# Optimization experiments

Measured on AMD Instinct MI355X. Metric: run time of the kernel, lower is better.

The kernel has to match this reference:

```python
import jax, jax.numpy as jnp
import numpy as np

N_NODES = 100000


def _gcn_layer(h, W, b, src, dst, norm, n):
    # h: [N, Fin] -> transform then normalized scatter-add aggregation
    h = h @ W                                   # [N, Fout]
    msg = h[src] * norm[:, None]                # [E', Fout] gather + scale
    out = jax.ops.segment_sum(msg, dst, num_segments=n)  # scatter-add
    return out + b


def setup_inputs() -> dict:
    key = jax.random.key(0)
    k1, k2, k3, k4 = jax.random.split(key, 4)
    N, F_IN, HID, C, E = N_NODES, 512, 128, 40, 1600000
    x = jax.random.normal(k1, (N, F_IN), dtype=jnp.float32)
    edge_index = jax.random.randint(k2, (2, E), 0, N, dtype=jnp.int64)
    W1 = jax.random.normal(k3, (F_IN, HID), dtype=jnp.float32) * (1.0 / np.sqrt(F_IN))
    b1 = jnp.zeros((HID,), dtype=jnp.float32)
    W2 = jax.random.normal(k4, (HID, C), dtype=jnp.float32) * (1.0 / np.sqrt(HID))
    b2 = jnp.zeros((C,), dtype=jnp.float32)
    return {"x": x, "edge_index": edge_index, "W1": W1, "b1": b1, "W2": W2, "b2": b2}


def reference(x, edge_index, W1, b1, W2, b2):
    n = x.shape[0]
    # add self-loops (GCNConv default)
    loop = jnp.arange(n, dtype=edge_index.dtype)
    src = jnp.concatenate([edge_index[0], loop])
    dst = jnp.concatenate([edge_index[1], loop])
    # symmetric normalization: deg counted on destination (in-degree, incl. self-loop)
    deg = jax.ops.segment_sum(jnp.ones_like(dst, dtype=x.dtype), dst, num_segments=n)
    dis = jnp.where(deg > 0, jax.lax.rsqrt(deg), 0.0)  # deg^{-1/2}
    norm = dis[src] * dis[dst]                          # per-edge weight

    h = jax.nn.relu(_gcn_layer(x, W1, b1, src, dst, norm, n))
    # dropout: identity in eval mode (training=False)
    h = _gcn_layer(h, W2, b2, src, dst, norm, n)
    return jax.nn.log_softmax(h, axis=1)
```

## Files before the change

### kernel.cpp

```cpp
#include <hip/hip_runtime.h>
#include <hip/hip_bf16.h>


#define F_IN 512
#define HID  128
#define NC   40

typedef __attribute__((ext_vector_type(8))) short bf16x8;
typedef __attribute__((ext_vector_type(4))) float f32x4v;

__device__ __forceinline__ ushort f2bf(float f) {
    union { float f; unsigned u; } x; x.f = f;
    unsigned r = x.u + 0x7FFFu + ((x.u >> 16) & 1u);
    return (ushort)(r >> 16);
}
__device__ __forceinline__ float bf2f(ushort u) {
    return __uint_as_float((unsigned)u << 16);
}

__global__ void count_deg(const int* __restrict__ dst, int E, unsigned* __restrict__ cnt) {
    int t = blockIdx.x * blockDim.x + threadIdx.x;
    if (t < E) atomicAdd(&cnt[dst[t]], 1u);
}

__global__ __launch_bounds__(1024) void scan_block(const unsigned* __restrict__ cnt,
                                                   unsigned* __restrict__ offs,
                                                   unsigned* __restrict__ bsums,
                                                   float* __restrict__ dis, int N) {
    __shared__ unsigned s[1024];
    int tid = threadIdx.x;
    int i = blockIdx.x * 1024 + tid;
    unsigned v = (i < N) ? cnt[i] : 0u;
    if (i < N) dis[i] = rsqrtf((float)v + 1.0f);
    s[tid] = v;
    __syncthreads();
    #pragma unroll
    for (int d = 1; d < 1024; d <<= 1) {
        unsigned t = (tid >= d) ? s[tid - d] : 0u;
        __syncthreads();
        s[tid] += t;
        __syncthreads();
    }
    if (i < N) offs[i] = s[tid] - v;
    if (tid == 1023) bsums[blockIdx.x] = s[1023];
}

__global__ __launch_bounds__(1024) void scan_bsums(unsigned* __restrict__ bsums, int nb) {
    __shared__ unsigned s[1024];
    int tid = threadIdx.x;
    unsigned v = (tid < nb) ? bsums[tid] : 0u;
    s[tid] = v;
    __syncthreads();
    #pragma unroll
    for (int d = 1; d < 1024; d <<= 1) {
        unsigned t = (tid >= d) ? s[tid - d] : 0u;
        __syncthreads();
        s[tid] += t;
        __syncthreads();
    }
    if (tid < nb) bsums[tid] = s[tid] - v;
}

__global__ __launch_bounds__(1024) void scan_add(unsigned* __restrict__ offs,
                                                 const unsigned* __restrict__ bsums,
                                                 int N, unsigned total) {
    int i = blockIdx.x * 1024 + threadIdx.x;
    if (i < N) offs[i] += bsums[blockIdx.x];
    if (i == 0) offs[N] = total;
}

__global__ void fill_csr(const int* __restrict__ src, const int* __restrict__ dst,
                         const unsigned* __restrict__ offs, unsigned* __restrict__ cursor,
                         int* __restrict__ col, int E) {
    int t = blockIdx.x * blockDim.x + threadIdx.x;
    if (t >= E) return;
    int s = src[t], d = dst[t];
    unsigned pos = offs[d] + atomicAdd(&cursor[d], 1u);
    col[pos] = s;
}

__global__ void packW(const float* __restrict__ W1, const float* __restrict__ W2,
                      ushort* __restrict__ W1p, ushort* __restrict__ W2p) {
    int t = blockIdx.x * 256 + threadIdx.x;
    if (t < 65536) {
        int j = t & 7, n = (t >> 3) & 127, kb = (t >> 10) & 3, s = t >> 12;
        int k = s * 32 + kb * 8 + j;
        W1p[t] = f2bf(W1[(size_t)k * HID + n]);
    } else {
        int q = t - 65536;
        if (q < 6144) {
            int j = q & 7;
            int i2 = q >> 3;
            int n = i2 % 48;
            int i3 = i2 / 48;
            int kb = i3 & 3, ks = i3 >> 2;
            int k = ks * 32 + kb * 8 + j;
            float v = (n < NC) ? W2[(size_t)k * NC + n] : 0.f;
            W2p[q] = f2bf(v);
        }
    }
}

__global__ __launch_bounds__(256) void gemm1_mfma(const float* __restrict__ A,
                                                  const ushort* __restrict__ Bp,
                                                  const float* __restrict__ dis,
                                                  ushort* __restrict__ C, int N) {
    __shared__ __align__(16) ushort As[2][64 * 40];
    __shared__ __align__(16) ushort Bs[2][4096];
    const int tid  = threadIdx.x;
    const int wave = tid >> 6;
    const int lane = tid & 63;
    const int quad = lane >> 4;
    const int mr   = lane & 15;
    const int bm   = blockIdx.x * 64;

    const int sr = tid >> 2;
    const int sq = tid & 3;
    const bool srow_ok = (bm + sr) < N;
    const float* aptr = A + (size_t)(bm + sr) * F_IN + sq * 8;

    f32x4v acc[8];
    #pragma unroll
    for (int t = 0; t < 8; t++) acc[t] = (f32x4v){0.f, 0.f, 0.f, 0.f};

    float4 av0, av1;
    uint4  bv0, bv1;
    const float4 z4 = make_float4(0.f, 0.f, 0.f, 0.f);

    av0 = srow_ok ? *(const float4*)(aptr)     : z4;
    av1 = srow_ok ? *(const float4*)(aptr + 4) : z4;
    bv0 = ((const uint4*)Bp)[tid];
    bv1 = ((const uint4*)Bp)[tid + 256];
    {
        __align__(16) ushort ta[8];
        ta[0]=f2bf(av0.x); ta[1]=f2bf(av0.y); ta[2]=f2bf(av0.z); ta[3]=f2bf(av0.w);
        ta[4]=f2bf(av1.x); ta[5]=f2bf(av1.y); ta[6]=f2bf(av1.z); ta[7]=f2bf(av1.w);
        *(uint4*)&As[0][sr * 40 + sq * 8] = *(const uint4*)ta;
        ((uint4*)Bs[0])[tid] = bv0;
        ((uint4*)Bs[0])[tid + 256] = bv1;
    }
    __syncthreads();

    for (int s = 0; s < 16; s++) {
        if (s < 15) {
            av0 = srow_ok ? *(const float4*)(aptr + (s + 1) * 32)     : z4;
            av1 = srow_ok ? *(const float4*)(aptr + (s + 1) * 32 + 4) : z4;
            const uint4* bp = (const uint4*)(Bp + (size_t)(s + 1) * 4096);
            bv0 = bp[tid];
            bv1 = bp[tid + 256];
        }
        {
            const ushort* ab = As[s & 1];
            const ushort* bb = Bs[s & 1] + quad * 1024;
            bf16x8 a = *(const bf16x8*)&ab[(wave * 16 + mr) * 40 + quad * 8];
            #pragma unroll
            for (int t = 0; t < 8; t++) {
                bf16x8 b = *(const bf16x8*)&bb[(t * 16 + mr) * 8];
                acc[t] = __builtin_amdgcn_mfma_f32_16x16x32_bf16(a, b, acc[t], 0, 0, 0);
            }
        }
        if (s < 15) {
            __align__(16) ushort ta[8];
            ta[0]=f2bf(av0.x); ta[1]=f2bf(av0.y); ta[2]=f2bf(av0.z); ta[3]=f2bf(av0.w);
            ta[4]=f2bf(av1.x); ta[5]=f2bf(av1.y); ta[6]=f2bf(av1.z); ta[7]=f2bf(av1.w);
            int nb = (s + 1) & 1;
            *(uint4*)&As[nb][sr * 40 + sq * 8] = *(const uint4*)ta;
            ((uint4*)Bs[nb])[tid] = bv0;
            ((uint4*)Bs[nb])[tid + 256] = bv1;
        }
        __syncthreads();
    }

    #pragma unroll
    for (int rr = 0; rr < 4; rr++) {
        int row = bm + wave * 16 + quad * 4 + rr;
        if (row < N) {
            float ds = dis[row];
            #pragma unroll
            for (int t = 0; t < 8; t++)
                C[(size_t)row * HID + t * 16 + mr] = f2bf(acc[t][rr] * ds);
        }
    }
}

__global__ __launch_bounds__(256) void agg1_k(const ushort* __restrict__ h,
                                              const int* __restrict__ col,
                                              const unsigned* __restrict__ offs,
                                              const float* __restrict__ dis,
                                              ushort* __restrict__ out, int N) {
    int node = blockIdx.x * 16 + (threadIdx.x >> 4);
    if (node >= N) return;
    int lane = threadIdx.x & 15;
    const size_t coff = (size_t)lane * 8;
    float a[8];
    {
        uint4 v = *(const uint4*)(h + (size_t)node * HID + coff);
        const ushort* u = (const ushort*)&v;
        #pragma unroll
        for (int j = 0; j < 8; j++) a[j] = bf2f(u[j]);
    }
    unsigned p0 = offs[node], p1 = offs[node + 1];
    unsigned p = p0;
    for (; p + 8 <= p1; p += 8) {
        int s0 = col[p],   s1 = col[p+1], s2 = col[p+2], s3 = col[p+3];
        int s4 = col[p+4], s5 = col[p+5], s6 = col[p+6], s7 = col[p+7];
        uint4 v0 = *(const uint4*)(h + (size_t)s0 * HID + coff);
        uint4 v1 = *(const uint4*)(h + (size_t)s1 * HID + coff);
        uint4 v2 = *(const uint4*)(h + (size_t)s2 * HID + coff);
        uint4 v3 = *(const uint4*)(h + (size_t)s3 * HID + coff);
        uint4 v4 = *(const uint4*)(h + (size_t)s4 * HID + coff);
        uint4 v5 = *(const uint4*)(h + (size_t)s5 * HID + coff);
        uint4 v6 = *(const uint4*)(h + (size_t)s6 * HID + coff);
        uint4 v7 = *(const uint4*)(h + (size_t)s7 * HID + coff);
        const ushort* u0 = (const ushort*)&v0;
        const ushort* u1 = (const ushort*)&v1;
        const ushort* u2 = (const ushort*)&v2;
        const ushort* u3 = (const ushort*)&v3;
        const ushort* u4 = (const ushort*)&v4;
        const ushort* u5 = (const ushort*)&v5;
        const ushort* u6 = (const ushort*)&v6;
        const ushort* u7 = (const ushort*)&v7;
        #pragma unroll
        for (int j = 0; j < 8; j++) {
            float t0 = bf2f(u0[j]) + bf2f(u1[j]);
            float t1 = bf2f(u2[j]) + bf2f(u3[j]);
            float t2 = bf2f(u4[j]) + bf2f(u5[j]);
            float t3 = bf2f(u6[j]) + bf2f(u7[j]);
            a[j] += (t0 + t1) + (t2 + t3);
        }
    }
    for (; p < p1; ++p) {
        int s = col[p];
        uint4 v = *(const uint4*)(h + (size_t)s * HID + coff);
        const ushort* u = (const ushort*)&v;
        #pragma unroll
        for (int j = 0; j < 8; j++) a[j] += bf2f(u[j]);
    }
    float dd = dis[node];
    __align__(16) ushort o[8];
    #pragma unroll
    for (int j = 0; j < 8; j++) o[j] = f2bf(a[j] * dd);
    *(uint4*)(out + (size_t)node * HID + coff) = *(const uint4*)o;
}

__global__ __launch_bounds__(256) void gemm2_mfma(const ushort* __restrict__ A,
                                                  const float* __restrict__ b1,
                                                  const ushort* __restrict__ W2p,
                                                  const float* __restrict__ dis,
                                                  ushort* __restrict__ h2, int N) {
    __shared__ __align__(16) ushort As[128 * 136];
    __shared__ __align__(16) ushort Bs[6144];
    const int tid = threadIdx.x;
    const int bm = blockIdx.x * 128;

    {
        const uint4* s4 = (const uint4*)W2p;
        uint4* d4 = (uint4*)Bs;
        #pragma unroll
        for (int i = 0; i < 3; i++) d4[tid + i * 256] = s4[tid + i * 256];
    }
    {
        const int r  = tid >> 1;
        const int hh = tid & 1;
        const int row = bm + r;
        const float* brow = b1 + hh * 64;
        if (row < N) {
            const ushort* arow = A + (size_t)row * HID + hh * 64;
            #pragma unroll
            for (int i = 0; i < 8; i++) {
                uint4 raw = *(const uint4*)(arow + i * 8);
                const ushort* u = (const ushort*)&raw;
                __align__(16) ushort tmp[8];
                #pragma unroll
                for (int j = 0; j < 8; j++)
                    tmp[j] = f2bf(fmaxf(bf2f(u[j]) + brow[i * 8 + j], 0.f));
                *(uint4*)&As[r * 136 + hh * 64 + i * 8] = *(const uint4*)tmp;
            }
        } else {
            #pragma unroll
            for (int i = 0; i < 8; i++) {
                uint4 zz = {0, 0, 0, 0};
                *(uint4*)&As[r * 136 + hh * 64 + i * 8] = zz;
            }
        }
    }
    __syncthreads();

    const int wave = tid >> 6;
    const int lane = tid & 63;
    const int quad = lane >> 4;
    const int mr   = lane & 15;
    f32x4v acc[2][3];
    #pragma unroll
    for (int i = 0; i < 2; i++)
        #pragma unroll
        for (int t = 0; t < 3; t++)
            acc[i][t] = (f32x4v){0.f, 0.f, 0.f, 0.f};
    #pragma unroll
    for (int ks = 0; ks < 4; ks++) {
        bf16x8 a0 = *(const bf16x8*)&As[(wave * 32 + mr) * 136 + ks * 32 + quad * 8];
        bf16x8 a1 = *(const bf16x8*)&As[(wave * 32 + 16 + mr) * 136 + ks * 32 + quad * 8];
        #pragma unroll
        for (int t = 0; t < 3; t++) {
            bf16x8 b = *(const bf16x8*)&Bs[((ks * 4 + quad) * 48 + t * 16 + mr) * 8];
            acc[0][t] = __builtin_amdgcn_mfma_f32_16x16x32_bf16(a0, b, acc[0][t], 0, 0, 0);
            acc[1][t] = __builtin_amdgcn_mfma_f32_16x16x32_bf16(a1, b, acc[1][t], 0, 0, 0);
        }
    }
    #pragma unroll
    for (int i = 0; i < 2; i++) {
        #pragma unroll
        for (int rr = 0; rr < 4; rr++) {
            int node = bm + wave * 32 + i * 16 + quad * 4 + rr;
            if (node < N) {
                float ds = dis[node];
                #pragma unroll
                for (int t = 0; t < 3; t++) {
                    int c = t * 16 + mr;
                    if (c < NC)
                        h2[(size_t)node * NC + c] = f2bf(acc[i][t][rr] * ds);
                }
            }
        }
    }
}

__global__ __launch_bounds__(256) void agg2_ls(const ushort* __restrict__ h2,
                                               const int* __restrict__ col,
                                               const unsigned* __restrict__ offs,
                                               const float* __restrict__ dis,
                                               const float* __restrict__ b2,
                                               float* __restrict__ out, int N) {
    int node = blockIdx.x * 32 + (threadIdx.x >> 3);
    if (node >= N) return;
    int lane = threadIdx.x & 7;
    const bool act = lane < 5;
    const size_t coff = (size_t)lane * 8;
    float a[8] = {};
    if (act) {
        uint4 v = *(const uint4*)(h2 + (size_t)node * NC + coff);
        const ushort* u = (const ushort*)&v;
        #pragma unroll
        for (int j = 0; j < 8; j++) a[j] = bf2f(u[j]);
    }
    unsigned p0 = offs[node], p1 = offs[node + 1];
    unsigned p = p0;
    for (; p + 4 <= p1; p += 4) {
        int s0 = col[p], s1 = col[p + 1], s2 = col[p + 2], s3 = col[p + 3];
        if (act) {
            uint4 v0 = *(const uint4*)(h2 + (size_t)s0 * NC + coff);
            uint4 v1 = *(const uint4*)(h2 + (size_t)s1 * NC + coff);
            uint4 v2 = *(const uint4*)(h2 + (size_t)s2 * NC + coff);
            uint4 v3 = *(const uint4*)(h2 + (size_t)s3 * NC + coff);
            const ushort* u0 = (const ushort*)&v0;
            const ushort* u1 = (const ushort*)&v1;
            const ushort* u2 = (const ushort*)&v2;
            const ushort* u3 = (const ushort*)&v3;
            #pragma unroll
            for (int j = 0; j < 8; j++)
                a[j] += (bf2f(u0[j]) + bf2f(u1[j])) + (bf2f(u2[j]) + bf2f(u3[j]));
        }
    }
    for (; p < p1; ++p) {
        int s = col[p];
        if (act) {
            uint4 v = *(const uint4*)(h2 + (size_t)s * NC + coff);
            const ushort* u = (const ushort*)&v;
            #pragma unroll
            for (int j = 0; j < 8; j++) a[j] += bf2f(u[j]);
        }
    }
    float dd = dis[node];
    float l[8];
    float m = -1e30f;
    if (act) {
        #pragma unroll
        for (int j = 0; j < 8; j++) {
            l[j] = a[j] * dd + b2[lane * 8 + j];
            m = fmaxf(m, l[j]);
        }
    }
    #pragma unroll
    for (int d = 1; d < 8; d <<= 1) m = fmaxf(m, __shfl_xor(m, d, 8));
    float s = 0.f;
    if (act) {
        #pragma unroll
        for (int j = 0; j < 8; j++) s += __expf(l[j] - m);
    }
    #pragma unroll
    for (int d = 1; d < 8; d <<= 1) s += __shfl_xor(s, d, 8);
    float lse = m + __logf(s);
    if (act) {
        float* op = out + (size_t)node * NC + lane * 8;
        *(float4*)op       = make_float4(l[0]-lse, l[1]-lse, l[2]-lse, l[3]-lse);
        *(float4*)(op + 4) = make_float4(l[4]-lse, l[5]-lse, l[6]-lse, l[7]-lse);
    }
}

extern "C" void kernel_launch(void* const* d_in, const int* in_sizes, int n_in,
                              void* d_out, int out_size, void* d_ws, size_t ws_size,
                              hipStream_t stream) {
    const float* x  = (const float*)d_in[0];
    const int*   ei = (const int*)d_in[1];
    const float* W1 = (const float*)d_in[2];
    const float* b1 = (const float*)d_in[3];
    const float* W2 = (const float*)d_in[4];
    const float* b2 = (const float*)d_in[5];
    float* out = (float*)d_out;

    const int N = in_sizes[0] / F_IN;
    const int E = in_sizes[1] / 2;
    const int* src = ei;
    const int* dst = ei + E;

    char* ws = (char*)d_ws;
    size_t o = 0;
    unsigned* cnt  = (unsigned*)(ws + o); o += (size_t)N * 4;
    unsigned* cur  = (unsigned*)(ws + o); o += (size_t)N * 4;
    float*    dis  = (float*)   (ws + o); o += (size_t)N * 4;
    unsigned* offs = (unsigned*)(ws + o); o += (size_t)(N + 4) * 4;
    unsigned* bsums= (unsigned*)(ws + o); o += 4096;
    int*      col  = (int*)     (ws + o); o += (size_t)E * 4;
    o = (o + 15) & ~(size_t)15;
    ushort*   W1p  = (ushort*)  (ws + o); o += (size_t)F_IN * HID * 2;
    o = (o + 15) & ~(size_t)15;
    ushort*   W2p  = (ushort*)  (ws + o); o += 6144 * 2;
    o = (o + 15) & ~(size_t)15;
    ushort*   h1   = (ushort*)  (ws + o); o += (size_t)N * HID * 2;
    o = (o + 15) & ~(size_t)15;
    ushort*   ag1  = (ushort*)  (ws + o); o += (size_t)N * HID * 2;
    o = (o + 15) & ~(size_t)15;
    ushort*   h2   = (ushort*)  (ws + o); o += (size_t)N * NC * 2;

    const int nb = (N + 1023) / 1024;

    hipMemsetAsync(cnt, 0, (size_t)N * 8, stream);
    count_deg<<<(E + 255) / 256, 256, 0, stream>>>(dst, E, cnt);
    scan_block<<<nb, 1024, 0, stream>>>(cnt, offs, bsums, dis, N);
    scan_bsums<<<1, 1024, 0, stream>>>(bsums, nb);
    scan_add<<<nb, 1024, 0, stream>>>(offs, bsums, N, (unsigned)E);
    fill_csr<<<(E + 255) / 256, 256, 0, stream>>>(src, dst, offs, cur, col, E);

    packW<<<(65536 + 6144 + 255) / 256, 256, 0, stream>>>(W1, W2, W1p, W2p);

    gemm1_mfma<<<(N + 63) / 64, 256, 0, stream>>>(x, W1p, dis, h1, N);
    agg1_k<<<(N + 15) / 16, 256, 0, stream>>>(h1, col, offs, dis, ag1, N);

    gemm2_mfma<<<(N + 127) / 128, 256, 0, stream>>>(ag1, b1, W2p, dis, h2, N);
    agg2_ls<<<(N + 31) / 32, 256, 0, stream>>>(h2, col, offs, dis, b2, out, N);
}
```

Measured before the change: 636.0 us.

## Load GEMM1 A operand directly into MFMA registers and deepen prefetch to two stages

The first-layer GEMM now has each lane load its own A fragment from global memory straight into registers and convert it to bf16 there. This removes the A shared-memory tile and its LDS write and read. The B tile and the A values are prefetched two k-steps ahead instead of one, to hide global latency better. In exchange, A global loads are less coalesced (each lane reads 32 bytes from a different row) and register pressure rises.

```diff
diff --git a/kernel.cpp b/kernel.cpp
--- a/kernel.cpp
+++ b/kernel.cpp
@@ -105,7 +105,6 @@
                                                   const ushort* __restrict__ Bp,
                                                   const float* __restrict__ dis,
                                                   ushort* __restrict__ C, int N) {
-    __shared__ __align__(16) ushort As[2][64 * 40];
     __shared__ __align__(16) ushort Bs[2][4096];
     const int tid  = threadIdx.x;
     const int wave = tid >> 6;
@@ -113,72 +112,69 @@
     const int quad = lane >> 4;
     const int mr   = lane & 15;
     const int bm   = blockIdx.x * 64;
-
-    const int sr = tid >> 2;
-    const int sq = tid & 3;
-    const bool srow_ok = (bm + sr) < N;
-    const float* aptr = A + (size_t)(bm + sr) * F_IN + sq * 8;
+    const int row  = bm + wave * 16 + mr;
+    const bool ok  = row < N;
+    const float* aptr = A + (size_t)(ok ? row : 0) * F_IN + quad * 8;
 
     f32x4v acc[8];
     #pragma unroll
     for (int t = 0; t < 8; t++) acc[t] = (f32x4v){0.f, 0.f, 0.f, 0.f};
 
-    float4 av0, av1;
-    uint4  bv0, bv1;
     const float4 z4 = make_float4(0.f, 0.f, 0.f, 0.f);
-
-    av0 = srow_ok ? *(const float4*)(aptr)     : z4;
-    av1 = srow_ok ? *(const float4*)(aptr + 4) : z4;
-    bv0 = ((const uint4*)Bp)[tid];
-    bv1 = ((const uint4*)Bp)[tid + 256];
+    float4 av[2][2];
+    uint4 bv0, bv1;
+
+    av[0][0] = ok ? *(const float4*)(aptr)      : z4;
+    av[0][1] = ok ? *(const float4*)(aptr + 4)  : z4;
+    av[1][0] = ok ? *(const float4*)(aptr + 32) : z4;
+    av[1][1] = ok ? *(const float4*)(aptr + 36) : z4;
+    ((uint4*)Bs[0])[tid]       = ((const uint4*)Bp)[tid];
+    ((uint4*)Bs[0])[tid + 256] = ((const uint4*)Bp)[tid + 256];
     {
+        const uint4* bp = (const uint4*)(Bp + 4096);
+        bv0 = bp[tid];
+        bv1 = bp[tid + 256];
+    }
+    __syncthreads();
+
+    for (int s = 0; s < 16; s++) {
+        float4 a0 = av[s & 1][0], a1 = av[s & 1][1];
         __align__(16) ushort ta[8];
-        ta[0]=f2bf(av0.x); ta[1]=f2bf(av0.y); ta[2]=f2bf(av0.z); ta[3]=f2bf(av0.w);
-        ta[4]=f2bf(av1.x); ta[5]=f2bf(av1.y); ta[6]=f2bf(av1.z); ta[7]=f2bf(av1.w);
-        *(uint4*)&As[0][sr * 40 + sq * 8] = *(const uint4*)ta;
-        ((uint4*)Bs[0])[tid] = bv0;
-        ((uint4*)Bs[0])[tid + 256] = bv1;
-    }
-    __syncthreads();
-
-    for (int s = 0; s < 16; s++) {
+        ta[0]=f2bf(a0.x); ta[1]=f2bf(a0.y); ta[2]=f2bf(a0.z); ta[3]=f2bf(a0.w);
+        ta[4]=f2bf(a1.x); ta[5]=f2bf(a1.y); ta[6]=f2bf(a1.z); ta[7]=f2bf(a1.w);
+        bf16x8 fa = *(const bf16x8*)ta;
         if (s < 15) {
-            av0 = srow_ok ? *(const float4*)(aptr + (s + 1) * 32)     : z4;
-            av1 = srow_ok ? *(const float4*)(aptr + (s + 1) * 32 + 4) : z4;
-            const uint4* bp = (const uint4*)(Bp + (size_t)(s + 1) * 4096);
+            ((uint4*)Bs[(s + 1) & 1])[tid]       = bv0;
+            ((uint4*)Bs[(s + 1) & 1])[tid + 256] = bv1;
+        }
+        if (s < 14) {
+            const uint4* bp = (const uint4*)(Bp + (size_t)(s + 2) * 4096);
             bv0 = bp[tid];
             bv1 = bp[tid + 256];
         }
+        if (s + 2 < 16) {
+            av[s & 1][0] = ok ? *(const float4*)(aptr + (s + 2) * 32)     : z4;
+            av[s & 1][1] = ok ? *(const float4*)(aptr + (s + 2) * 32 + 4) : z4;
+        }
         {
-            const ushort* ab = As[s & 1];
-            const ushort* bb = Bs[s & 1] + quad * 1024;
-            bf16x8 a = *(const bf16x8*)&ab[(wave * 16 + mr) * 40 + quad * 8];
+            const ushort* bb = Bs[s & 1] + quad * 1024 + mr * 8;
             #pragma unroll
             for (int t = 0; t < 8; t++) {
-                bf16x8 b = *(const bf16x8*)&bb[(t * 16 + mr) * 8];
-                acc[t] = __builtin_amdgcn_mfma_f32_16x16x32_bf16(a, b, acc[t], 0, 0, 0);
+                bf16x8 b = *(const bf16x8*)&bb[t * 128];
+                acc[t] = __builtin_amdgcn_mfma_f32_16x16x32_bf16(fa, b, acc[t], 0, 0, 0);
             }
         }
-        if (s < 15) {
-            __align__(16) ushort ta[8];
-            ta[0]=f2bf(av0.x); ta[1]=f2bf(av0.y); ta[2]=f2bf(av0.z); ta[3]=f2bf(av0.w);
-            ta[4]=f2bf(av1.x); ta[5]=f2bf(av1.y); ta[6]=f2bf(av1.z); ta[7]=f2bf(av1.w);
-            int nb = (s + 1) & 1;
-            *(uint4*)&As[nb][sr * 40 + sq * 8] = *(const uint4*)ta;
-            ((uint4*)Bs[nb])[tid] = bv0;
-            ((uint4*)Bs[nb])[tid + 256] = bv1;
-        }
         __syncthreads();
     }
 
     #pragma unroll
     for (int rr = 0; rr < 4; rr++) {
-        int row = bm + wave * 16 + quad * 4 + rr;
-        if (row < N) {
-            float ds = dis[row];
+        int r = bm + wave * 16 + quad * 4 + rr;
+        if (r < N) {
+            float ds = dis[r];
             #pragma unroll
             for (int t = 0; t < 8; t++)
-                C[(size_t)row * HID + t * 16 + mr] = f2bf(acc[t][rr] * ds);
+                C[(size_t)r * HID + t * 16 + mr] = f2bf(acc[t][rr] * ds);
         }
     }
 }
```

Result: no change. 647.8 us (+1.8%).
